# Kernel optimization log

Hardware: AMD Instinct MI355X
Metric: run time of the kernel (lower is better)

The kernel has to match this reference:

```python
import jax, jax.numpy as jnp
import numpy as np

N, E, G = 50000, 500000, 32
H, D = 4, 40  # heads, per-head dim; hidden = H*D = 160
HID, JK = H * D, 2 * H * D  # 160, 320


def setup_inputs() -> dict:
    key = jax.random.key(0)
    ks = jax.random.split(key, 32)
    s = 0.05
    inp = {
        'x': jax.random.normal(ks[0], (N, 5), jnp.float32),
        'edge_index': jax.random.randint(ks[1], (2, E), 0, N, jnp.int32).astype(jnp.int64),
        'edge_attr': jax.random.normal(ks[2], (E, 4), jnp.float32),
        'batch': jnp.sort(jax.random.randint(ks[3], (N,), 0, G, jnp.int32)).astype(jnp.int64),
        'W_in': jax.random.normal(ks[4], (5, HID), jnp.float32) * s,
        'b_in': jnp.zeros((HID,), jnp.float32),
        'Wq': jax.random.normal(ks[5], (2, HID, HID), jnp.float32) * s,
        'bq': jnp.zeros((2, HID), jnp.float32),
        'Wk': jax.random.normal(ks[6], (2, HID, HID), jnp.float32) * s,
        'bk': jnp.zeros((2, HID), jnp.float32),
        'Wv': jax.random.normal(ks[7], (2, HID, HID), jnp.float32) * s,
        'bv': jnp.zeros((2, HID), jnp.float32),
        'We': jax.random.normal(ks[8], (2, 4, HID), jnp.float32) * s,
        'be': jnp.zeros((2, HID), jnp.float32),
        'Wskip': jax.random.normal(ks[9], (2, HID, HID), jnp.float32) * s,
        'bskip': jnp.zeros((2, HID), jnp.float32),
        'Wbeta': jax.random.normal(ks[10], (2, 3 * HID, 1), jnp.float32) * s,
        'Wg1': jax.random.normal(ks[11], (JK, JK // 2), jnp.float32) * s,
        'bg1': jnp.zeros((JK // 2,), jnp.float32),
        'Wg2': jax.random.normal(ks[12], (JK // 2, 1), jnp.float32) * s,
        'bg2': jnp.zeros((1,), jnp.float32),
        'Wh1': jax.random.normal(ks[13], (JK, JK), jnp.float32) * s,
        'bh1': jnp.zeros((JK,), jnp.float32),
        'Wh2': jax.random.normal(ks[14], (JK, 6), jnp.float32) * s,
        'bh2': jnp.zeros((6,), jnp.float32),
    }
    return inp


def _transformer_conv(h, src, dst, edge_attr, Wq, bq, Wk, bk, Wv, bv, We, be, Wskip, bskip, Wbeta):
    n = h.shape[0]
    q = (h @ Wq + bq).reshape(n, H, D)
    k = (h @ Wk + bk).reshape(n, H, D)
    v = (h @ Wv + bv).reshape(n, H, D)
    e = (edge_attr @ We + be).reshape(-1, H, D)   # [E,H,D]
    k_e = k[src] + e                              # key with edge feature
    v_e = v[src] + e                              # value with edge feature
    alpha = jnp.einsum('ehd,ehd->eh', q[dst], k_e) / jnp.sqrt(jnp.float32(D))  # [E,H]
    # segment softmax over incoming edges of each destination node
    amax = jax.ops.segment_max(alpha, dst, num_segments=n)
    ex = jnp.exp(alpha - amax[dst])
    denom = jax.ops.segment_sum(ex, dst, num_segments=n)
    a = ex / denom[dst]                           # [E,H]
    out = jax.ops.segment_sum(v_e * a[..., None], dst, num_segments=n).reshape(n, H * D)
    # beta gate with skip connection
    r = h @ Wskip + bskip
    beta = jax.nn.sigmoid(jnp.concatenate([out, r, out - r], axis=-1) @ Wbeta)  # [n,1]
    return beta * r + (1.0 - beta) * out


def reference(x, edge_index, edge_attr, batch, W_in, b_in, Wq, bq, Wk, bk, Wv, bv,
              We, be, Wskip, bskip, Wbeta, Wg1, bg1, Wg2, bg2, Wh1, bh1, Wh2, bh2):
    src, dst = edge_index[0], edge_index[1]
    h = x @ W_in + b_in
    xs = []
    for l in range(2):
        h = _transformer_conv(h, src, dst, edge_attr, Wq[l], bq[l], Wk[l], bk[l],
                              Wv[l], bv[l], We[l], be[l], Wskip[l], bskip[l], Wbeta[l])
        xs.append(h)
    xc = jnp.concatenate(xs, axis=-1)             # JumpingKnowledge 'cat' -> [N,320]
    # AttentionalAggregation: gate MLP + segment softmax over graphs
    gate = jax.nn.relu(xc @ Wg1 + bg1) @ Wg2 + bg2  # [N,1]
    gmax = jax.ops.segment_max(gate, batch, num_segments=G)
    ge = jnp.exp(gate - gmax[batch])
    gden = jax.ops.segment_sum(ge, batch, num_segments=G)
    att = ge / gden[batch]
    pooled = jax.ops.segment_sum(att * xc, batch, num_segments=G)  # [G,320]
    out = jax.nn.relu(pooled @ Wh1 + bh1) @ Wh2 + bh2              # [G,6]
    return out.reshape(-1, 2, 3)
```

## Files before the change

### kernel.cpp

```cpp
#include <hip/hip_runtime.h>
#include <math.h>
#include <stddef.h>

#define NHEAD 4
#define DHEAD 40
#define HIDW 160
#define JKW 320
#define NGRAPH 32
#define BCAP 64
#define BCOLS 768
#define BREAL 660

typedef __attribute__((ext_vector_type(8))) short short8;
typedef __attribute__((ext_vector_type(4))) float f32x4;
typedef __attribute__((ext_vector_type(2))) float f32x2;
typedef __fp16 h2 __attribute__((ext_vector_type(2)));
typedef int i32x4 __attribute__((ext_vector_type(4)));
typedef i32x4 i32x4_a4 __attribute__((aligned(4)));

__device__ inline unsigned short f2bf(float x){
  unsigned u = __float_as_uint(x);
  u += 0x7fff + ((u >> 16) & 1);
  return (unsigned short)(u >> 16);
}
__device__ inline float bf2f(unsigned short h){
  return __uint_as_float(((unsigned)h) << 16);
}
__device__ inline float fdot2(h2 a, h2 b, float c){
  return __builtin_amdgcn_fdot2(a, b, c, false);
}
__device__ inline h2 pk(float a, float b){
  return __builtin_amdgcn_cvt_pkrtz(a, b);
}
union HU { h2 h; int i; unsigned u; float f; };
__device__ inline h2 shfl_h2(h2 v, int xm){
  HU u; u.h = v; u.i = __shfl_xor(u.i, xm); return u.h;
}
__device__ inline h2 asH2(unsigned i){ HU u; u.u = i; return u.h; }

#if __has_builtin(__builtin_amdgcn_cvt_pk_f16_fp8)
__device__ inline h2 cvt8(int s){ return __builtin_amdgcn_cvt_pk_f16_fp8((short)s); }
#else
__device__ inline h2 cvt8(int s){
  f32x2 t = __builtin_amdgcn_cvt_pk_f32_fp8(s, false);
  return pk(t.x, t.y);
}
#endif

__device__ inline int lbound(const int* __restrict__ b, int N, int g){
  int lo = 0, hi = N;
  while (lo < hi){ int mid = (lo + hi) >> 1; if (b[mid] < g) lo = mid + 1; else hi = mid; }
  return lo;
}

__global__ __launch_bounds__(256) void k_pre(const float* __restrict__ x, const float* __restrict__ W_in,
                                             const float* __restrict__ b_in, unsigned short* __restrict__ hb,
                                             const float* __restrict__ Wq, const float* __restrict__ Wk,
                                             const float* __restrict__ Wv, const float* __restrict__ Ws,
                                             const float* __restrict__ bq, const float* __restrict__ bk,
                                             const float* __restrict__ bv, const float* __restrict__ bs,
                                             const float* __restrict__ Wg1,
                                             const float* __restrict__ We, const float* __restrict__ be,
                                             unsigned short* __restrict__ Bth, float* __restrict__ bp,
                                             unsigned short* __restrict__ Btgh,
                                             int* __restrict__ cnt, float* __restrict__ gate,
                                             float* __restrict__ pooled, int N){
  const float qscale = 0.15811388300841898f;
  int NL = (N*20 + 255)/256;
  int bid = blockIdx.x, tid = threadIdx.x;
  if (bid < NL){
    int idx = bid*256 + tid;
    if (idx >= N*20) return;
    int n = idx / 20, j8 = (idx % 20)*8;
    const float* xr = x + n*5;
    float x0 = xr[0], x1 = xr[1], x2 = xr[2], x3 = xr[3], x4 = xr[4];
    float v[8];
    #pragma unroll
    for (int u = 0; u < 8; ++u) v[u] = b_in[j8+u];
    #pragma unroll
    for (int c = 0; c < 5; ++c){
      float xc = (c==0)?x0:(c==1)?x1:(c==2)?x2:(c==3)?x3:x4;
      const float4 wa = *(const float4*)(W_in + c*HIDW + j8);
      const float4 wb = *(const float4*)(W_in + c*HIDW + j8 + 4);
      v[0] += xc*wa.x; v[1] += xc*wa.y; v[2] += xc*wa.z; v[3] += xc*wa.w;
      v[4] += xc*wb.x; v[5] += xc*wb.y; v[6] += xc*wb.z; v[7] += xc*wb.w;
    }
    short8 o;
    #pragma unroll
    for (int u = 0; u < 8; ++u) o[u] = (short)f2bf(v[u]);
    *(short8*)(hb + (size_t)n*JKW + j8) = o;
  } else if (bid < NL + 1166){
    int idx = (bid - NL)*256 + tid;
    if (idx < 2*BCOLS*160){
      int l = idx / (BCOLS*160), r = idx % (BCOLS*160);
      int i = r / BCOLS, j = r % BCOLS;
      unsigned short outv;
      if (j < 640){
        int sel = j / HIDW, jj = j % HIDW;
        const float* W = (sel==0) ? Wq : (sel==1) ? Wk : (sel==2) ? Wv : Ws;
        outv = f2bf(W[(size_t)l*25600 + i*HIDW + jj]);
      } else if (j < BREAL){
        int c = j - 640, h = c / 5, rr = c % 5;
        const float* wqr = Wq + (size_t)l*25600 + i*HIDW + 40*h;
        const float* xr  = (rr < 4) ? (We + l*640 + rr*160 + 40*h) : (be + l*160 + 40*h);
        float s = 0.f;
        #pragma unroll
        for (int d = 0; d < 40; ++d) s += wqr[d]*xr[d];
        outv = f2bf(s * qscale);
      } else outv = 0;
      Bth[(size_t)l*(BCOLS*160) + (size_t)j*160 + i] = outv;
    } else if (idx < 2*BCOLS*160 + 51200){
      int r = idx - 2*BCOLS*160;
      int j = r / 320, i = r % 320;
      Btgh[(size_t)j*320 + i] = f2bf(Wg1[(size_t)i*160 + j]);
    } else if (idx < 2*BCOLS*160 + 51200 + 2*BCOLS){
      int r = idx - (2*BCOLS*160 + 51200);
      int l = r / BCOLS, j = r % BCOLS;
      float bvv;
      if (j < 640){
        int sel = j / HIDW, jj = j % HIDW;
        const float* b2 = (sel==0) ? bq : (sel==1) ? bk : (sel==2) ? bv : bs;
        bvv = b2[l*160 + jj];
      } else if (j < BREAL){
        int c = j - 640, h = c / 5, rr = c % 5;
        const float* bqr = bq + l*160 + 40*h;
        const float* xr  = (rr < 4) ? (We + l*640 + rr*160 + 40*h) : (be + l*160 + 40*h);
        float s = 0.f;
        #pragma unroll
        for (int d = 0; d < 40; ++d) s += bqr[d]*xr[d];
        bvv = s * qscale;
      } else bvv = 0.f;
      bp[l*BCOLS + j] = bvv;
    }
  } else {
    int idx = (bid - NL - 1166)*256 + tid;
    if (idx < N){ cnt[idx] = 0; gate[idx] = 0.f; }
    if (idx < NGRAPH*JKW) pooled[idx] = 0.f;
  }
}

__global__ __launch_bounds__(256) void k_fill(const int* __restrict__ dst, const int* __restrict__ src,
                                              const float* __restrict__ edge_attr, int E,
                                              int* __restrict__ cnt, uint4* __restrict__ edges){
  int e = blockIdx.x*256 + threadIdx.x;
  if (e < E){
    int d = dst[e];
    int p = atomicAdd(&cnt[d], 1);
    if (p < BCAP){
      float4 ea = *(const float4*)(edge_attr + (size_t)e*4);
      HU a, b; a.h = pk(ea.x, ea.y); b.h = pk(ea.z, ea.w);
      edges[(size_t)d*BCAP + p] = make_uint4((unsigned)src[e], a.u, b.u, 0u);
    }
  }
}

#define BSTR 40
#define BSTR1 164
template<int NSUB, int MODE>
__global__ __launch_bounds__(256) void k_mgemm(const unsigned short* __restrict__ A, int lda,
                                               const unsigned short* __restrict__ Bh,
                                               const float* __restrict__ bias,
                                               _Float16* __restrict__ qh,
                                               unsigned char* __restrict__ kv8,
                                               _Float16* __restrict__ rskip,
                                               float* __restrict__ qwb,
                                               const float* __restrict__ Wg2,
                                               float* __restrict__ gate,
                                               int M, int K){
  __shared__ short sBh[(MODE==1) ? (16*NSUB*BSTR1) : (2*16*NSUB*BSTR)];
  int tid = threadIdx.x;
  int wv = tid >> 6, lane = tid & 63;
  int quad = lane >> 4, l16 = lane & 15;

  int P = gridDim.x, MBy = gridDim.y;
  int bid = blockIdx.y * P + blockIdx.x;
  int fullRows = (MBy >> 3) << 3;
  int rowB, panel;
  if (bid < fullRows * P){
    int group = bid / (8*P), rem = bid % (8*P);
    rowB  = group*8 + (rem & 7);
    panel = rem >> 3;
  } else {
    int rem = bid - fullRows*P;
    int R = MBy - fullRows;
    panel = rem / R;
    rowB  = fullRows + rem % R;
  }
  int m0 = rowB*128 + wv*32;
  int col0 = panel * (16*NSUB);

  int ar0 = m0 + l16;      if (ar0 >= M) ar0 = M - 1;
  int ar1 = m0 + 16 + l16; if (ar1 >= M) ar1 = M - 1;
  const unsigned short* Ap0 = A + (size_t)ar0*lda + quad*8;
  const unsigned short* Ap1 = A + (size_t)ar1*lda + quad*8;

  f32x4 acc[2][NSUB];
  #pragma unroll
  for (int g = 0; g < 2; ++g)
    #pragma unroll
    for (int s = 0; s < NSUB; ++s) acc[g][s] = (f32x4){0.f,0.f,0.f,0.f};

  if constexpr (MODE == 1){
    for (int u = tid; u < 16*NSUB*20; u += 256){
      int col = u / 20, q = u % 20;
      *(short8*)(&sBh[col*BSTR1 + q*8]) =
        *(const short8*)(Bh + (size_t)(col0 + col)*K + q*8);
    }
    __syncthreads();
    #pragma unroll
    for (int kk = 0; kk < 5; ++kk){
      int k0 = kk << 5;
      short8 ah0 = *(const short8*)(Ap0 + k0);
      short8 ah1 = *(const short8*)(Ap1 + k0);
      #pragma unroll
      for (int s = 0; s < NSUB; ++s){
        short8 bh = *(const short8*)(&sBh[(s*16 + l16)*BSTR1 + k0 + quad*8]);
        acc[0][s] = __builtin_amdgcn_mfma_f32_16x16x32_bf16(bh, ah0, acc[0][s], 0, 0, 0);
        acc[1][s] = __builtin_amdgcn_mfma_f32_16x16x32_bf16(bh, ah1, acc[1][s], 0, 0, 0);
      }
    }
  } else {
    const int CH = K >> 5;
    for (int u = tid; u < 16*NSUB*4; u += 256){
      int col = u >> 2, q4 = u & 3;
      *(short8*)(&sBh[col*BSTR + q4*8]) =
        *(const short8*)(Bh + (size_t)(col0 + col)*K + q4*8);
    }
    __syncthreads();
    int buf = 0;
    for (int kk = 0; kk < CH; ++kk){
      int k0 = kk << 5;
      if (kk + 1 < CH){
        int kn = k0 + 32;
        for (int u = tid; u < 16*NSUB*4; u += 256){
          int col = u >> 2, q4 = u & 3;
          *(short8*)(&sBh[(buf^1)*16*NSUB*BSTR + col*BSTR + q4*8]) =
            *(const short8*)(Bh + (size_t)(col0 + col)*K + kn + q4*8);
        }
      }
      short8 ah0 = *(const short8*)(Ap0 + k0);
      short8 ah1 = *(const short8*)(Ap1 + k0);
      #pragma unroll
      for (int s = 0; s < NSUB; ++s){
        short8 bh = *(const short8*)(&sBh[buf*16*NSUB*BSTR + (s*16 + l16)*BSTR + quad*8]);
        acc[0][s] = __builtin_amdgcn_mfma_f32_16x16x32_bf16(bh, ah0, acc[0][s], 0, 0, 0);
        acc[1][s] = __builtin_amdgcn_mfma_f32_16x16x32_bf16(bh, ah1, acc[1][s], 0, 0, 0);
      }
      __syncthreads();
      buf ^= 1;
    }
  }

  const float qscale = 0.15811388300841898f;
  if (MODE == 1){
    #pragma unroll
    for (int g = 0; g < 2; ++g){
      int row = m0 + g*16 + l16;
      if (row >= M) continue;
      #pragma unroll
      for (int s = 0; s < NSUB; ++s){
        int col4 = col0 + s*16 + quad*4;
        int sel = col4 / 160, cc4 = col4 % 160;
        const float4 bv = *(const float4*)(bias + col4);
        float v0 = acc[g][s][0] + bv.x;
        float v1 = acc[g][s][1] + bv.y;
        float v2 = acc[g][s][2] + bv.z;
        float v3 = acc[g][s][3] + bv.w;
        if (sel == 0){
          HU a, b; a.h = pk(v0*qscale, v1*qscale); b.h = pk(v2*qscale, v3*qscale);
          *(uint2*)(qh + (size_t)row*160 + cc4) = make_uint2(a.u, b.u);
        } else if (sel == 3){
          HU a, b; a.h = pk(v0, v1); b.h = pk(v2, v3);
          *(uint2*)(rskip + (size_t)row*160 + cc4) = make_uint2(a.u, b.u);
        } else if (sel >= 4){
          if (col4 < BREAL){
            float4 o4; o4.x = v0; o4.y = v1; o4.z = v2; o4.w = v3;
            *(float4*)(qwb + (size_t)row*20 + (col4 - 640)) = o4;
          }
        } else {
          int slot = (cc4/40)*4 + (cc4%40)/10, j = cc4%10;
          int off = (sel==2) ? 10 : 0;
          unsigned short e01 = (unsigned short)(__builtin_amdgcn_cvt_pk_fp8_f32(v0, v1, 0, false) & 0xffff);
          unsigned short e23 = (unsigned short)(__builtin_amdgcn_cvt_pk_fp8_f32(v2, v3, 0, false) & 0xffff);
          unsigned char* base = kv8 + (size_t)row*320;
          if (j <= 6){
            *(unsigned short*)(base + slot*20 + off + j)     = e01;
            *(unsigned short*)(base + slot*20 + off + j + 2) = e23;
          } else {
            *(unsigned short*)(base + slot*20 + off + 8)     = e01;
            *(unsigned short*)(base + (slot+1)*20 + off + 0) = e23;
          }
        }
      }
    }
  } else {
    float vg0 = 0.f, vg1 = 0.f;
    #pragma unroll
    for (int s = 0; s < NSUB; ++s){
      int col4 = col0 + s*16 + quad*4;
      const float4 bv = *(const float4*)(bias + col4);
      const float4 wg = *(const float4*)(Wg2 + col4);
      vg0 += fmaxf(acc[0][s][0]+bv.x,0.f)*wg.x + fmaxf(acc[0][s][1]+bv.y,0.f)*wg.y
           + fmaxf(acc[0][s][2]+bv.z,0.f)*wg.z + fmaxf(acc[0][s][3]+bv.w,0.f)*wg.w;
      vg1 += fmaxf(acc[1][s][0]+bv.x,0.f)*wg.x + fmaxf(acc[1][s][1]+bv.y,0.f)*wg.y
           + fmaxf(acc[1][s][2]+bv.z,0.f)*wg.z + fmaxf(acc[1][s][3]+bv.w,0.f)*wg.w;
    }
    vg0 += __shfl_xor(vg0, 16); vg0 += __shfl_xor(vg0, 32);
    vg1 += __shfl_xor(vg1, 16); vg1 += __shfl_xor(vg1, 32);
    if (quad == 0){
      int row0 = m0 + l16, row1 = m0 + 16 + l16;
      if (row0 < M) gate[row0] = vg0;
      if (row1 < M) gate[row1] = vg1;
    }
  }
}

__global__ __launch_bounds__(256) void k_attn(const _Float16* __restrict__ qh,
                                              const unsigned char* __restrict__ kv8,
                                              const _Float16* __restrict__ rskip,
                                              const float* __restrict__ qwb,
                                              const uint4* __restrict__ edges,
                                              const int* __restrict__ cnt,
                                              const float* __restrict__ We, const float* __restrict__ be,
                                              const float* __restrict__ Wb,
                                              unsigned short* __restrict__ hb,
                                              int loff, int N){
  int tid = threadIdx.x;
  int grp = tid >> 4;
  int n = blockIdx.x*16 + grp;
  bool valid = (n < N);
  int nn = valid ? n : (N-1);
  int w = tid & 15;
  int hh = w & 3, t = w >> 2;
  int cbase = DHEAD*hh + 10*t;
  int slot = hh*4 + t;

  h2 qh2[5];
  {
    const unsigned* qp = (const unsigned*)(qh + (size_t)nn*160 + cbase);
    #pragma unroll
    for (int i = 0; i < 5; ++i) qh2[i] = asH2(qp[i]);
  }
  const float* qwp = qwb + (size_t)nn*20 + hh*5;
  float qw0 = qwp[0], qw1 = qwp[1], qw2 = qwp[2], qw3 = qwp[3], qb = qwp[4];
  h2 qw01 = pk(qw0, qw1), qw23 = pk(qw2, qw3);

  float ssum = 0.f;
  h2 zh = pk(0.f, 0.f);
  h2 acch[5], sah[2];
  #pragma unroll
  for (int i = 0; i < 5; ++i) acch[i] = zh;
  sah[0] = zh; sah[1] = zh;

  int deg = 0;
  if (valid){ deg = cnt[nn]; if (deg > BCAP) deg = BCAP; }
  int st = nn*BCAP;

  uint4 r0 = make_uint4(0,0,0,0), r1 = make_uint4(0,0,0,0);
  uint4 r2 = make_uint4(0,0,0,0), r3 = make_uint4(0,0,0,0);
  i32x4 k0v = {0,0,0,0}, k1v = {0,0,0,0}; int k0e = 0, k1e = 0;
  if (deg > 0) r0 = edges[st];
  if (deg > 1) r1 = edges[st+1];
  if (deg > 2) r2 = edges[st+2];
  if (deg > 3) r3 = edges[st+3];
  if (deg > 0){
    const unsigned char* kp = kv8 + (size_t)r0.x*320 + slot*20;
    k0v = *(const i32x4_a4*)kp; k0e = *(const int*)(kp+16);
  }
  if (deg > 1){
    const unsigned char* kp = kv8 + (size_t)r1.x*320 + slot*20;
    k1v = *(const i32x4_a4*)kp; k1e = *(const int*)(kp+16);
  }

  for (int e = 0; e < deg; e += 2){
    uint4 n0 = make_uint4(0,0,0,0), n1 = make_uint4(0,0,0,0);
    if (e + 4 < deg) n0 = edges[st + e + 4];
    if (e + 5 < deg) n1 = edges[st + e + 5];
    i32x4 k2v = {0,0,0,0}, k3v = {0,0,0,0}; int k2e = 0, k3e = 0;
    if (e + 2 < deg){
      const unsigned char* kp = kv8 + (size_t)r2.x*320 + slot*20;
      k2v = *(const i32x4_a4*)kp; k2e = *(const int*)(kp+16);
    }
    if (e + 3 < deg){
      const unsigned char* kp = kv8 + (size_t)r3.x*320 + slot*20;
      k3v = *(const i32x4_a4*)kp; k3e = *(const int*)(kp+16);
    }
    bool v1 = (e + 1 < deg);
    h2 ea00 = asH2(r0.y), ea01 = asH2(r0.z);
    h2 ea10 = asH2(r1.y), ea11 = asH2(r1.z);
    float p0 = 0.f, p1 = 0.f;
    p0 = fdot2(qh2[0], cvt8(k0v.x), p0);       p1 = fdot2(qh2[0], cvt8(k1v.x), p1);
    p0 = fdot2(qh2[1], cvt8(k0v.x >> 16), p0); p1 = fdot2(qh2[1], cvt8(k1v.x >> 16), p1);
    p0 = fdot2(qh2[2], cvt8(k0v.y), p0);       p1 = fdot2(qh2[2], cvt8(k1v.y), p1);
    p0 = fdot2(qh2[3], cvt8(k0v.y >> 16), p0); p1 = fdot2(qh2[3], cvt8(k1v.y >> 16), p1);
    p0 = fdot2(qh2[4], cvt8(k0v.z), p0);       p1 = fdot2(qh2[4], cvt8(k1v.z), p1);
    p0 += __shfl_xor(p0, 4);                   p1 += __shfl_xor(p1, 4);
    p0 += __shfl_xor(p0, 8);                   p1 += __shfl_xor(p1, 8);
    p0 += qb;                                  p1 += qb;
    p0 = fdot2(ea00, qw01, p0);                p1 = fdot2(ea10, qw01, p1);
    p0 = fdot2(ea01, qw23, p0);                p1 = fdot2(ea11, qw23, p1);

    float ex0 = __expf(p0);
    float ex1 = v1 ? __expf(p1) : 0.f;
    ssum += ex0;
    ssum += ex1;
    h2 eh0 = pk(ex0, ex0), eh1 = pk(ex1, ex1);
    acch[0] += cvt8(k0v.z >> 16)*eh0;  acch[0] += cvt8(k1v.z >> 16)*eh1;
    acch[1] += cvt8(k0v.w)*eh0;        acch[1] += cvt8(k1v.w)*eh1;
    acch[2] += cvt8(k0v.w >> 16)*eh0;  acch[2] += cvt8(k1v.w >> 16)*eh1;
    acch[3] += cvt8(k0e)*eh0;          acch[3] += cvt8(k1e)*eh1;
    acch[4] += cvt8(k0e >> 16)*eh0;    acch[4] += cvt8(k1e >> 16)*eh1;
    sah[0] += ea00*eh0;                sah[0] += ea10*eh1;
    sah[1] += ea01*eh0;                sah[1] += ea11*eh1;

    r0 = r2; r1 = r3; r2 = n0; r3 = n1;
    k0v = k2v; k0e = k2e; k1v = k3v; k1e = k3e;
  }

  {
    float inv = (ssum > 0.f) ? 1.f/ssum : 0.f;
    float sw0 = (float)sah[0].x*inv, sw1 = (float)sah[0].y*inv;
    float sw2 = (float)sah[1].x*inv, sw3 = (float)sah[1].y*inv;
    float bterm = (ssum > 0.f) ? 1.f : 0.f;

    const unsigned* rpu = (const unsigned*)(rskip + (size_t)nn*160 + cbase);
    float o[10];
    float part = 0.f;
    #pragma unroll
    for (int i = 0; i < 5; ++i){
      int c = cbase + 2*i;
      float o0 = (float)acch[i].x*inv + sw0*We[c]   + sw1*We[160+c] + sw2*We[320+c] + sw3*We[480+c] + bterm*be[c];
      float o1 = (float)acch[i].y*inv + sw0*We[c+1] + sw1*We[161+c] + sw2*We[321+c] + sw3*We[481+c] + bterm*be[c+1];
      HU u; u.u = rpu[i];
      float r0f = (float)u.h.x, r1f = (float)u.h.y;
      part += o0*Wb[c]   + r0f*Wb[160+c] + (o0-r0f)*Wb[320+c];
      part += o1*Wb[c+1] + r1f*Wb[161+c] + (o1-r1f)*Wb[321+c];
      o[2*i] = o0; o[2*i+1] = o1;
    }
    part += __shfl_xor(part, 1); part += __shfl_xor(part, 2);
    part += __shfl_xor(part, 4); part += __shfl_xor(part, 8);
    float beta = 1.f/(1.f + __expf(-part));
    if (valid){
      unsigned* hp32 = (unsigned*)(hb + (size_t)nn*JKW + loff);
      #pragma unroll
      for (int i = 0; i < 5; ++i){
        HU u; u.u = rpu[i];
        float r0f = (float)u.h.x, r1f = (float)u.h.y;
        unsigned lo = f2bf(beta*r0f + (1.f-beta)*o[2*i]);
        unsigned hi = f2bf(beta*r1f + (1.f-beta)*o[2*i+1]);
        hp32[cbase/2 + i] = lo | (hi << 16);
      }
    }
  }
}

__global__ __launch_bounds__(256) void k_gatt(float* __restrict__ gate, const int* __restrict__ batch, int N){
  __shared__ float sm[256];
  int g = blockIdx.x, j = threadIdx.x;
  int lo = lbound(batch, N, g), hi = lbound(batch, N, g+1);
  if (hi <= lo) return;
  float m = -INFINITY;
  for (int i = lo + j; i < hi; i += 256) m = fmaxf(m, gate[i]);
  sm[j] = m; __syncthreads();
  #pragma unroll
  for (int off = 128; off; off >>= 1){
    if (j < off) sm[j] = fmaxf(sm[j], sm[j+off]);
    __syncthreads();
  }
  float gm = sm[0]; __syncthreads();
  float s = 0.f;
  for (int i = lo + j; i < hi; i += 256) s += __expf(gate[i] - gm);
  sm[j] = s; __syncthreads();
  #pragma unroll
  for (int off = 128; off; off >>= 1){
    if (j < off) sm[j] += sm[j+off];
    __syncthreads();
  }
  float dg = sm[0];
  float invd = (dg > 0.f) ? 1.f/dg : 0.f;
  for (int i = lo + j; i < hi; i += 256) gate[i] = __expf(gate[i] - gm) * invd;
}

__global__ __launch_bounds__(320) void k_pool(const unsigned short* __restrict__ hb, const float* __restrict__ gate,
                                              const int* __restrict__ batch, int N,
                                              float* __restrict__ pooled){
  int g = blockIdx.x, part = blockIdx.y, j = threadIdx.x;
  int lo = lbound(batch, N, g), hi = lbound(batch, N, g+1);
  int len = hi - lo;
  if (len <= 0) return;
  int chunk = (len + (int)gridDim.y - 1) / (int)gridDim.y;
  int a = lo + part*chunk;
  int bnd = a + chunk; if (bnd > hi) bnd = hi;
  if (a >= bnd) return;
  float acc = 0.f;
  #pragma unroll 2
  for (int n = a; n < bnd; ++n){
    acc += gate[n] * bf2f(hb[(size_t)n*JKW + j]);
  }
  atomicAdd(&pooled[g*JKW + j], acc);
}

__global__ __launch_bounds__(320) void k_head(const float* __restrict__ pooled, const float* __restrict__ Wh1,
                                              const float* __restrict__ bh1, const float* __restrict__ Wh2,
                                              const float* __restrict__ bh2, float* __restrict__ out){
  __shared__ float p[320];
  __shared__ float t[320];
  int g = blockIdx.x, tid = threadIdx.x;
  p[tid] = pooled[g*JKW + tid]; __syncthreads();
  float a = bh1[tid];
  for (int i = 0; i < 320; ++i) a += p[i]*Wh1[i*JKW + tid];
  t[tid] = fmaxf(a, 0.f); __syncthreads();
  if (tid < 6){
    float o = bh2[tid];
    for (int j = 0; j < 320; ++j) o += t[j]*Wh2[j*6 + tid];
    out[g*6 + tid] = o;
  }
}

extern "C" void kernel_launch(void* const* d_in, const int* in_sizes, int n_in,
                              void* d_out, int out_size, void* d_ws, size_t ws_size,
                              hipStream_t stream){
  (void)n_in; (void)out_size; (void)ws_size;
  const float* x        = (const float*)d_in[0];
  const int*   eidx     = (const int*)d_in[1];
  const float* edge_attr= (const float*)d_in[2];
  const int*   batch    = (const int*)d_in[3];
  const float* W_in     = (const float*)d_in[4];
  const float* b_in     = (const float*)d_in[5];
  const float* Wq       = (const float*)d_in[6];
  const float* bq       = (const float*)d_in[7];
  const float* Wk       = (const float*)d_in[8];
  const float* bk       = (const float*)d_in[9];
  const float* Wv       = (const float*)d_in[10];
  const float* bv       = (const float*)d_in[11];
  const float* We       = (const float*)d_in[12];
  const float* be       = (const float*)d_in[13];
  const float* Wsk      = (const float*)d_in[14];
  const float* bsk      = (const float*)d_in[15];
  const float* Wb       = (const float*)d_in[16];
  const float* Wg1      = (const float*)d_in[17];
  const float* bg1      = (const float*)d_in[18];
  const float* Wg2      = (const float*)d_in[19];
  const float* Wh1      = (const float*)d_in[21];
  const float* bh1      = (const float*)d_in[22];
  const float* Wh2      = (const float*)d_in[23];
  const float* bh2      = (const float*)d_in[24];

  const int N = in_sizes[0] / 5;
  const int E = in_sizes[1] / 2;
  float* out = (float*)d_out;

  char* w = (char*)d_ws;
  auto alloc = [&](size_t bytes)->char*{ char* p = w; w += (bytes + 255) & ~(size_t)255; return p; };
  unsigned short* hb = (unsigned short*)alloc((size_t)N*JKW*2);
  _Float16* qh  = (_Float16*)alloc((size_t)N*160*2);
  unsigned char* kv8 = (unsigned char*)alloc((size_t)N*320);
  _Float16* rskip = (_Float16*)alloc((size_t)N*160*2);
  float* qwb    = (float*)alloc((size_t)N*20*4);
  unsigned short* Bth  = (unsigned short*)alloc((size_t)2*BCOLS*160*2);
  unsigned short* Btgh = (unsigned short*)alloc((size_t)160*320*2);
  float* bpack  = (float*)alloc((size_t)2*BCOLS*4);
  int*   cnt    = (int*)alloc((size_t)N*4);
  uint4* edges  = (uint4*)alloc((size_t)N*BCAP*16);
  float* gate   = (float*)alloc((size_t)N*4);
  float* pooled = (float*)alloc(NGRAPH*JKW*4);

  const int* srcI = eidx;
  const int* dstI = eidx + E;

  const int NL = (N*20 + 255)/256;
  const int NZ = (N + 255)/256;
  k_pre<<<NL + 1166 + NZ, 256, 0, stream>>>(x, W_in, b_in, hb,
                                            Wq, Wk, Wv, Wsk, bq, bk, bv, bsk, Wg1, We, be,
                                            Bth, bpack, Btgh, cnt, gate, pooled, N);

  const int eb = (E + 255)/256;
  k_fill<<<eb, 256, 0, stream>>>(dstI, srcI, edge_attr, E, cnt, edges);

  const int MB128 = (N + 127)/128;
  for (int l = 0; l < 2; ++l){
    dim3 g1(6, MB128);
    k_mgemm<8,1><<<g1, 256, 0, stream>>>(hb, JKW, Bth + (size_t)l*(BCOLS*160), bpack + l*BCOLS,
                                         qh, kv8, rskip, qwb, nullptr, nullptr, N, HIDW);
    k_attn<<<(N + 15)/16, 256, 0, stream>>>(qh, kv8, rskip, qwb, edges, cnt,
                                            We + l*640, be + l*160, Wb + l*480, hb, l*HIDW, N);
  }

  k_mgemm<10,2><<<dim3(1, MB128), 256, 0, stream>>>(hb, JKW, Btgh, bg1, nullptr, nullptr, nullptr, nullptr,
                                                    Wg2, gate, N, JKW);

  k_gatt<<<NGRAPH, 256, 0, stream>>>(gate, batch, N);
  dim3 g3(NGRAPH, 32);
  k_pool<<<g3, 320, 0, stream>>>(hb, gate, batch, N, pooled);
  k_head<<<NGRAPH, 320, 0, stream>>>(pooled, Wh1, bh1, Wh2, bh2, out);
}
```

Baseline: 402.0 us.

## Keep QKV weight panel in registers and loop each block over row tiles

Result: slower. 414.3 us (+3.0%).

```diff
diff --git a/kernel.cpp b/kernel.cpp
--- a/kernel.cpp
+++ b/kernel.cpp
@@ -10,6 +10,7 @@
 #define BCAP 64
 #define BCOLS 768
 #define BREAL 660
+#define MITER 4
 
 typedef __attribute__((ext_vector_type(8))) short short8;
 typedef __attribute__((ext_vector_type(4))) float f32x4;
@@ -155,7 +156,6 @@
 }
 
 #define BSTR 40
-#define BSTR1 164
 template<int NSUB, int MODE>
 __global__ __launch_bounds__(256) void k_mgemm(const unsigned short* __restrict__ A, int lda,
                                                const unsigned short* __restrict__ Bh,
@@ -167,59 +167,139 @@
                                                const float* __restrict__ Wg2,
                                                float* __restrict__ gate,
                                                int M, int K){
-  __shared__ short sBh[(MODE==1) ? (16*NSUB*BSTR1) : (2*16*NSUB*BSTR)];
   int tid = threadIdx.x;
   int wv = tid >> 6, lane = tid & 63;
   int quad = lane >> 4, l16 = lane & 15;
-
-  int P = gridDim.x, MBy = gridDim.y;
-  int bid = blockIdx.y * P + blockIdx.x;
-  int fullRows = (MBy >> 3) << 3;
-  int rowB, panel;
-  if (bid < fullRows * P){
-    int group = bid / (8*P), rem = bid % (8*P);
-    rowB  = group*8 + (rem & 7);
-    panel = rem >> 3;
+  const float qscale = 0.15811388300841898f;
+
+  if constexpr (MODE == 1){
+    int P = gridDim.x, G = gridDim.y;
+    int bid = blockIdx.y * P + blockIdx.x;
+    int fullG = (G >> 3) << 3;
+    int grpB, panel;
+    if (bid < fullG * P){
+      int gg = bid / (8*P), rem = bid % (8*P);
+      grpB  = gg*8 + (rem & 7);
+      panel = rem >> 3;
+    } else {
+      int rem = bid - fullG*P;
+      int R = G - fullG;
+      panel = rem / R;
+      grpB  = fullG + rem % R;
+    }
+    int col0 = panel * (16*NSUB);
+
+    short8 breg[NSUB][5];
+    const unsigned short* Bp = Bh + (size_t)(col0 + l16)*K + quad*8;
+    #pragma unroll
+    for (int s = 0; s < NSUB; ++s)
+      #pragma unroll
+      for (int kk = 0; kk < 5; ++kk)
+        breg[s][kk] = *(const short8*)(Bp + (size_t)s*16*K + kk*32);
+
+    float4 bvc[NSUB];
+    #pragma unroll
+    for (int s = 0; s < NSUB; ++s)
+      bvc[s] = *(const float4*)(bias + col0 + s*16 + quad*4);
+
+    for (int it = 0; it < MITER; ++it){
+      int rowB = grpB*MITER + it;
+      int m0 = rowB*128 + wv*32;
+      if (m0 >= M && rowB > 0) break;
+      int ar0 = m0 + l16;      if (ar0 >= M) ar0 = M - 1;
+      int ar1 = m0 + 16 + l16; if (ar1 >= M) ar1 = M - 1;
+      const unsigned short* Ap0 = A + (size_t)ar0*lda + quad*8;
+      const unsigned short* Ap1 = A + (size_t)ar1*lda + quad*8;
+
+      f32x4 acc[2][NSUB];
+      #pragma unroll
+      for (int g = 0; g < 2; ++g)
+        #pragma unroll
+        for (int s = 0; s < NSUB; ++s) acc[g][s] = (f32x4){0.f,0.f,0.f,0.f};
+
+      #pragma unroll
+      for (int kk = 0; kk < 5; ++kk){
+        int k0 = kk << 5;
+        short8 ah0 = *(const short8*)(Ap0 + k0);
+        short8 ah1 = *(const short8*)(Ap1 + k0);
+        #pragma unroll
+        for (int s = 0; s < NSUB; ++s){
+          acc[0][s] = __builtin_amdgcn_mfma_f32_16x16x32_bf16(breg[s][kk], ah0, acc[0][s], 0, 0, 0);
+          acc[1][s] = __builtin_amdgcn_mfma_f32_16x16x32_bf16(breg[s][kk], ah1, acc[1][s], 0, 0, 0);
+        }
+      }
+
+      #pragma unroll
+      for (int g = 0; g < 2; ++g){
+        int row = m0 + g*16 + l16;
+        if (row >= M) continue;
+        #pragma unroll
+        for (int s = 0; s < NSUB; ++s){
+          int col4 = col0 + s*16 + quad*4;
+          int sel = col4 / 160, cc4 = col4 % 160;
+          const float4 bv = bvc[s];
+          float v0 = acc[g][s][0] + bv.x;
+          float v1 = acc[g][s][1] + bv.y;
+          float v2 = acc[g][s][2] + bv.z;
+          float v3 = acc[g][s][3] + bv.w;
+          if (sel == 0){
+            HU a, b; a.h = pk(v0*qscale, v1*qscale); b.h = pk(v2*qscale, v3*qscale);
+            *(uint2*)(qh + (size_t)row*160 + cc4) = make_uint2(a.u, b.u);
+          } else if (sel == 3){
+            HU a, b; a.h = pk(v0, v1); b.h = pk(v2, v3);
+            *(uint2*)(rskip + (size_t)row*160 + cc4) = make_uint2(a.u, b.u);
+          } else if (sel >= 4){
+            if (col4 < BREAL){
+              float4 o4; o4.x = v0; o4.y = v1; o4.z = v2; o4.w = v3;
+              *(float4*)(qwb + (size_t)row*20 + (col4 - 640)) = o4;
+            }
+          } else {
+            int slot = (cc4/40)*4 + (cc4%40)/10, j = cc4%10;
+            int off = (sel==2) ? 10 : 0;
+            unsigned short e01 = (unsigned short)(__builtin_amdgcn_cvt_pk_fp8_f32(v0, v1, 0, false) & 0xffff);
+            unsigned short e23 = (unsigned short)(__builtin_amdgcn_cvt_pk_fp8_f32(v2, v3, 0, false) & 0xffff);
+            unsigned char* base = kv8 + (size_t)row*320;
+            if (j <= 6){
+              *(unsigned short*)(base + slot*20 + off + j)     = e01;
+              *(unsigned short*)(base + slot*20 + off + j + 2) = e23;
+            } else {
+              *(unsigned short*)(base + slot*20 + off + 8)     = e01;
+              *(unsigned short*)(base + (slot+1)*20 + off + 0) = e23;
+            }
+          }
+        }
+      }
+    }
   } else {
-    int rem = bid - fullRows*P;
-    int R = MBy - fullRows;
-    panel = rem / R;
-    rowB  = fullRows + rem % R;
-  }
-  int m0 = rowB*128 + wv*32;
-  int col0 = panel * (16*NSUB);
-
-  int ar0 = m0 + l16;      if (ar0 >= M) ar0 = M - 1;
-  int ar1 = m0 + 16 + l16; if (ar1 >= M) ar1 = M - 1;
-  const unsigned short* Ap0 = A + (size_t)ar0*lda + quad*8;
-  const unsigned short* Ap1 = A + (size_t)ar1*lda + quad*8;
-
-  f32x4 acc[2][NSUB];
-  #pragma unroll
-  for (int g = 0; g < 2; ++g)
-    #pragma unroll
-    for (int s = 0; s < NSUB; ++s) acc[g][s] = (f32x4){0.f,0.f,0.f,0.f};
-
-  if constexpr (MODE == 1){
-    for (int u = tid; u < 16*NSUB*20; u += 256){
-      int col = u / 20, q = u % 20;
-      *(short8*)(&sBh[col*BSTR1 + q*8]) =
-        *(const short8*)(Bh + (size_t)(col0 + col)*K + q*8);
-    }
-    __syncthreads();
-    #pragma unroll
-    for (int kk = 0; kk < 5; ++kk){
-      int k0 = kk << 5;
-      short8 ah0 = *(const short8*)(Ap0 + k0);
-      short8 ah1 = *(const short8*)(Ap1 + k0);
+    __shared__ short sBh[2*16*NSUB*BSTR];
+    int P = gridDim.x, MBy = gridDim.y;
+    int bid = blockIdx.y * P + blockIdx.x;
+    int fullRows = (MBy >> 3) << 3;
+    int rowB, panel;
+    if (bid < fullRows * P){
+      int group = bid / (8*P), rem = bid % (8*P);
+      rowB  = group*8 + (rem & 7);
+      panel = rem >> 3;
+    } else {
+      int rem = bid - fullRows*P;
+      int R = MBy - fullRows;
+      panel = rem / R;
+      rowB  = fullRows + rem % R;
+    }
+    int m0 = rowB*128 + wv*32;
+    int col0 = panel * (16*NSUB);
+
+    int ar0 = m0 + l16;      if (ar0 >= M) ar0 = M - 1;
+    int ar1 = m0 + 16 + l16; if (ar1 >= M) ar1 = M - 1;
+    const unsigned short* Ap0 = A + (size_t)ar0*lda + quad*8;
+    const unsigned short* Ap1 = A + (size_t)ar1*lda + quad*8;
+
+    f32x4 acc[2][NSUB];
+    #pragma unroll
+    for (int g = 0; g < 2; ++g)
       #pragma unroll
-      for (int s = 0; s < NSUB; ++s){
-        short8 bh = *(const short8*)(&sBh[(s*16 + l16)*BSTR1 + k0 + quad*8]);
-        acc[0][s] = __builtin_amdgcn_mfma_f32_16x16x32_bf16(bh, ah0, acc[0][s], 0, 0, 0);
-        acc[1][s] = __builtin_amdgcn_mfma_f32_16x16x32_bf16(bh, ah1, acc[1][s], 0, 0, 0);
-      }
-    }
-  } else {
+      for (int s = 0; s < NSUB; ++s) acc[g][s] = (f32x4){0.f,0.f,0.f,0.f};
+
     const int CH = K >> 5;
     for (int u = tid; u < 16*NSUB*4; u += 256){
       int col = u >> 2, q4 = u & 3;
@@ -249,51 +329,7 @@
       __syncthreads();
       buf ^= 1;
     }
-  }
-
-  const float qscale = 0.15811388300841898f;
-  if (MODE == 1){
-    #pragma unroll
-    for (int g = 0; g < 2; ++g){
-      int row = m0 + g*16 + l16;
-      if (row >= M) continue;
-      #pragma unroll
-      for (int s = 0; s < NSUB; ++s){
-        int col4 = col0 + s*16 + quad*4;
-        int sel = col4 / 160, cc4 = col4 % 160;
-        const float4 bv = *(const float4*)(bias + col4);
-        float v0 = acc[g][s][0] + bv.x;
-        float v1 = acc[g][s][1] + bv.y;
-        float v2 = acc[g][s][2] + bv.z;
-        float v3 = acc[g][s][3] + bv.w;
-        if (sel == 0){
-          HU a, b; a.h = pk(v0*qscale, v1*qscale); b.h = pk(v2*qscale, v3*qscale);
-          *(uint2*)(qh + (size_t)row*160 + cc4) = make_uint2(a.u, b.u);
-        } else if (sel == 3){
-          HU a, b; a.h = pk(v0, v1); b.h = pk(v2, v3);
-          *(uint2*)(rskip + (size_t)row*160 + cc4) = make_uint2(a.u, b.u);
-        } else if (sel >= 4){
-          if (col4 < BREAL){
-            float4 o4; o4.x = v0; o4.y = v1; o4.z = v2; o4.w = v3;
-            *(float4*)(qwb + (size_t)row*20 + (col4 - 640)) = o4;
-          }
-        } else {
-          int slot = (cc4/40)*4 + (cc4%40)/10, j = cc4%10;
-          int off = (sel==2) ? 10 : 0;
-          unsigned short e01 = (unsigned short)(__builtin_amdgcn_cvt_pk_fp8_f32(v0, v1, 0, false) & 0xffff);
-          unsigned short e23 = (unsigned short)(__builtin_amdgcn_cvt_pk_fp8_f32(v2, v3, 0, false) & 0xffff);
-          unsigned char* base = kv8 + (size_t)row*320;
-          if (j <= 6){
-            *(unsigned short*)(base + slot*20 + off + j)     = e01;
-            *(unsigned short*)(base + slot*20 + off + j + 2) = e23;
-          } else {
-            *(unsigned short*)(base + slot*20 + off + 8)     = e01;
-            *(unsigned short*)(base + (slot+1)*20 + off + 0) = e23;
-          }
-        }
-      }
-    }
-  } else {
+
     float vg0 = 0.f, vg1 = 0.f;
     #pragma unroll
     for (int s = 0; s < NSUB; ++s){
@@ -578,9 +614,10 @@
   k_fill<<<eb, 256, 0, stream>>>(dstI, srcI, edge_attr, E, cnt, edges);
 
   const int MB128 = (N + 127)/128;
+  const int GRP = (MB128 + MITER - 1)/MITER;
   for (int l = 0; l < 2; ++l){
-    dim3 g1(6, MB128);
-    k_mgemm<8,1><<<g1, 256, 0, stream>>>(hb, JKW, Bth + (size_t)l*(BCOLS*160), bpack + l*BCOLS,
+    dim3 g1(11, GRP);
+    k_mgemm<4,1><<<g1, 256, 0, stream>>>(hb, JKW, Bth + (size_t)l*(BCOLS*160), bpack + l*BCOLS,
                                          qh, kv8, rskip, qwb, nullptr, nullptr, N, HIDW);
     k_attn<<<(N + 15)/16, 256, 0, stream>>>(qh, kv8, rskip, qwb, edges, cnt,
                                             We + l*640, be + l*160, Wb + l*480, hb, l*HIDW, N);
```
